# Performance work log

Measured on AMD Instinct MI355X. Metric: run time of the kernel, lower is better.

The kernel has to match this reference:

```python
import jax, jax.numpy as jnp
import numpy as np
import math

D_MODEL = 64
N_HEAD = 8
BATCH = 16
NTOK = 511  # pads to 512 in original torch code; padn = 1 > 0


def setup_inputs() -> dict:
    key = jax.random.key(0)
    ks = jax.random.split(key, 4)
    scl = 0.005
    x = jax.random.normal(ks[0], (BATCH, NTOK, D_MODEL), jnp.float32)
    wq_w = scl * jax.random.normal(ks[1], (N_HEAD * D_MODEL, D_MODEL + 1), jnp.float32)
    wq_w = wq_w.at[:, -1].set(0.0)  # bias column zeroed at init
    wv_w = scl * jax.random.normal(ks[2], (N_HEAD * D_MODEL, D_MODEL + 1), jnp.float32)
    wv_w = wv_w.at[:, -1].set(0.0)
    wk = scl * jnp.ones((N_HEAD, D_MODEL), jnp.float32)
    fanout_w = scl * jax.random.normal(ks[3], (D_MODEL, D_MODEL + 1), jnp.float32)
    fanout_w = fanout_w.at[:, -1].set(0.0)
    return {"x": x, "wq_w": wq_w, "wv_w": wv_w, "wk": wk, "fanout_w": fanout_w}


def _linear_m(w, x):
    # LinearM: w[:, :-1] is weight, w[:, -1] is bias
    return jnp.einsum('oi,bti->bto', w[:, :-1], x) + w[:, -1]


def _l1_logits(q, k):
    # q, k: [b, t, h, w]. Returns [b, s(key), d(query), h] =
    #   -(1/sqrt(w)) * sum_w |q[b,d,h,w] - k[b,s,h,w]|
    # Scan over the width axis so we never materialize a [b,t,t,h,w] tensor.
    b, t, h, w = q.shape
    scale = 1.0 / math.sqrt(w)
    qw = jnp.moveaxis(q, -1, 0)  # [w, b, t, h]
    kw = jnp.moveaxis(k, -1, 0)

    def body(acc, qk):
        qi, ki = qk  # each [b, t, h]
        return acc + jnp.abs(qi[:, None, :, :] - ki[:, :, None, :]), None

    acc0 = jnp.zeros((b, t, t, h), q.dtype)
    acc, _ = jax.lax.scan(body, acc0, (qw, kw))
    return -acc * scale


def reference(x, wq_w, wv_w, wk, fanout_w):
    b, t, dm = x.shape
    q = _linear_m(wq_w, x).reshape(b, t, N_HEAD, D_MODEL)
    v = _linear_m(wv_w, x).reshape(b, t, N_HEAD, D_MODEL)
    # k: x broadcast over heads, elementwise-gated by wk
    k = x[:, :, None, :] * wk[None, None, :, :]  # [b, t, h, w]
    logits = _l1_logits(q, k)  # [b, s, d, h]
    # Extra zero-logit 'sink' key row (the original zero-padded row with a[:,t,:,:]=0)
    sink = jnp.zeros((b, 1, t, N_HEAD), logits.dtype)
    logits = jnp.concatenate([logits, sink], axis=1)  # [b, t+1, d, h]
    a = jax.nn.softmax(logits, axis=1)[:, :t]  # softmax over keys+sink, drop sink
    # einsum 'bsdh,bshw->bdhw' then sum over h, fused:
    out = jnp.einsum('bsdh,bshw->bdw', a, v)  # [b, t, d_model]
    y = jax.nn.relu(out)  # module's self.gelu is actually nn.ReLU()
    y = _linear_m(fanout_w, y)
    return x + y
```

## Files before the change

kernel.cpp:

```cpp
#include <hip/hip_runtime.h>
#include <stdint.h>


#define B  16
#define H  8
#define T  511

typedef __fp16 f16x2 __attribute__((ext_vector_type(2)));
typedef __fp16 f16x8 __attribute__((ext_vector_type(8)));
typedef float  f32x4 __attribute__((ext_vector_type(4)));

#if __has_builtin(__builtin_amdgcn_exp2f)
#define EXP2F(x) __builtin_amdgcn_exp2f(x)
#else
#define EXP2F(x) exp2f(x)
#endif

__device__ __forceinline__ uint32_t SAD(uint32_t a, uint32_t b, uint32_t c) {
#if __has_builtin(__builtin_amdgcn_sad_u8)
  return __builtin_amdgcn_sad_u8(a, b, c);
#else
  uint32_t d;
  asm("v_sad_u8 %0, %1, %2, %3" : "=v"(d) : "v"(a), "v"(b), "v"(c));
  return d;
#endif
}

__device__ __forceinline__ uint32_t PKRTZ(float a, float b) {
  f16x2 r = __builtin_amdgcn_cvt_pkrtz(a, b);
  return __builtin_bit_cast(uint32_t, r);
}

__device__ __forceinline__ uint32_t quantu8(float v) {
  float q = __builtin_rintf(__builtin_fmaf(v, 256.f, 128.f));
  q = fminf(fmaxf(q, 0.f), 255.f);
  return (uint32_t)(int)q;
}

__global__ void wtrans_kernel(const float* __restrict__ wq, const float* __restrict__ wv,
                              const float* __restrict__ wf, float* __restrict__ wt,
                              float* __restrict__ bias, float* __restrict__ wft,
                              float* __restrict__ biasf) {
  const int idx = blockIdx.x * 256 + (int)threadIdx.x;
  if (idx < 64 * 1024) {
    const int k = idx >> 10, j = idx & 1023;
    const float* src = (j < 512) ? wq : wv;
    const int oc = j & 511;
    wt[idx] = src[oc * 65 + k];
    if (k == 0) bias[j] = src[oc * 65 + 64];
  } else if (idx < 64 * 1024 + 64 * 64) {
    const int r = idx - 64 * 1024;
    const int k = r >> 6, w = r & 63;
    wft[r] = wf[w * 65 + k];
    if (k == 0) biasf[w] = wf[w * 65 + 64];
  }
}

__global__ void __launch_bounds__(256, 2) proj_kernel(
    const float* __restrict__ x, const float* __restrict__ wt,
    const float* __restrict__ bias, const float* __restrict__ wk,
    uint8_t* __restrict__ qq, _Float16* __restrict__ vt,
    uint8_t* __restrict__ kq) {
  __shared__ float xt[64][16];
  const int b = blockIdx.y, tc = blockIdx.x;
  const int t0 = tc * 16;
  const int tid = threadIdx.x;
  {
    const int tl = tid >> 4, k0 = (tid & 15) * 4;
    const int t = t0 + tl;
    float4 v = {0.f, 0.f, 0.f, 0.f};
    if (t < T) v = *(const float4*)(x + ((size_t)b * T + t) * 64 + k0);
    xt[k0 + 0][tl] = v.x; xt[k0 + 1][tl] = v.y;
    xt[k0 + 2][tl] = v.z; xt[k0 + 3][tl] = v.w;
  }
  __syncthreads();
  const int j0 = tid * 4;
  const float4 bs = *(const float4*)(bias + j0);
  float4 acc[16];
#pragma unroll
  for (int t = 0; t < 16; ++t) acc[t] = bs;
  for (int k = 0; k < 64; ++k) {
    const float4 w4 = *(const float4*)(wt + (size_t)k * 1024 + j0);
    const float4* xr = (const float4*)xt[k];
    const float4 xa = xr[0], xb = xr[1], xc = xr[2], xd = xr[3];
    const float xv[16] = {xa.x, xa.y, xa.z, xa.w, xb.x, xb.y, xb.z, xb.w,
                          xc.x, xc.y, xc.z, xc.w, xd.x, xd.y, xd.z, xd.w};
#pragma unroll
    for (int t = 0; t < 16; ++t) {
      acc[t].x = __builtin_fmaf(w4.x, xv[t], acc[t].x);
      acc[t].y = __builtin_fmaf(w4.y, xv[t], acc[t].y);
      acc[t].z = __builtin_fmaf(w4.z, xv[t], acc[t].z);
      acc[t].w = __builtin_fmaf(w4.w, xv[t], acc[t].w);
    }
  }
  const int oc = j0 & 511;
  const int hh = oc >> 6, w0 = oc & 63;
  const size_t bh = (size_t)b * H + hh;
  if (j0 < 512) {
#pragma unroll
    for (int t = 0; t < 16; ++t) {
      if (t0 + t < T) {
        const uint32_t u = quantu8(acc[t].x) | (quantu8(acc[t].y) << 8) |
                           (quantu8(acc[t].z) << 16) | (quantu8(acc[t].w) << 24);
        *(uint32_t*)(qq + (bh * T + (size_t)(t0 + t)) * 64 + w0) = u;
      }
    }
  } else {
#pragma unroll
    for (int i = 0; i < 4; ++i) {
      uint32_t u[8];
      const float* a = (const float*)acc;
#pragma unroll
      for (int m = 0; m < 8; ++m) u[m] = PKRTZ(a[4 * (2 * m) + i], a[4 * (2 * m + 1) + i]);
      _Float16* p = vt + (bh * 64 + (size_t)(w0 + i)) * 512 + t0;
      *(uint4*)(p)     = make_uint4(u[0], u[1], u[2], u[3]);
      *(uint4*)(p + 8) = make_uint4(u[4], u[5], u[6], u[7]);
    }
  }
  const int tk = tid >> 4, w4 = (tid & 15) * 4;
  if (t0 + tk < T) {
    const float xv0 = xt[w4 + 0][tk], xv1 = xt[w4 + 1][tk];
    const float xv2 = xt[w4 + 2][tk], xv3 = xt[w4 + 3][tk];
#pragma unroll
    for (int hh2 = 0; hh2 < H; ++hh2) {
      const float4 wkv = *(const float4*)(wk + hh2 * 64 + w4);
      const uint32_t u = quantu8(xv0 * wkv.x) | (quantu8(xv1 * wkv.y) << 8) |
                         (quantu8(xv2 * wkv.z) << 16) | (quantu8(xv3 * wkv.w) << 24);
      *(uint32_t*)(kq + (((size_t)b * H + hh2) * T + (size_t)(t0 + tk)) * 64 + w4) = u;
    }
  }
}

__global__ void __launch_bounds__(256, 4) attn_kernel(
    const uint8_t* __restrict__ qq, const uint8_t* __restrict__ kq,
    const _Float16* __restrict__ vt, _Float16* __restrict__ anum) {
  __shared__ uint4 klds[2048];
  const int qt = blockIdx.x, h = blockIdx.y, b = blockIdx.z;
  const int bh = b * H + h;
  const int tid = threadIdx.x;
  {
    const uint4* kg = (const uint4*)(kq + (size_t)bh * T * 64);
    for (int i = tid; i < T * 4; i += 256) klds[i] = kg[i];
  }
  const int wave = tid >> 6, lane = tid & 63;
  const int c = lane & 15, g = lane >> 4;
  const int qb = qt * 64 + wave * 16;
  const int q = qb + c;
  const int qsafe = q < T ? q : T - 1;
  const uint4* qp = (const uint4*)(qq + ((size_t)bh * T + qsafe) * 64);
  const uint4 q0 = qp[0], q1 = qp[1], q2 = qp[2], q3 = qp[3];
  const _Float16* vb = vt + (size_t)bh * 64 * 512;
  f32x4 acc0 = {0.f, 0.f, 0.f, 0.f}, acc1 = acc0, acc2 = acc0, acc3 = acc0;
  float den = 0.f;
  const float Cl = -0x1.715476p+0f / 2048.0f;
  __syncthreads();

  auto sadrow = [&](int s) -> float {
    const uint4* kp = klds + s * 4;
    const uint4 k0 = kp[0], k1 = kp[1], k2 = kp[2], k3 = kp[3];
    uint32_t a0 = 0, a1 = 0;
    a0 = SAD(q0.x, k0.x, a0); a0 = SAD(q0.y, k0.y, a0);
    a0 = SAD(q0.z, k0.z, a0); a0 = SAD(q0.w, k0.w, a0);
    a0 = SAD(q1.x, k1.x, a0); a0 = SAD(q1.y, k1.y, a0);
    a0 = SAD(q1.z, k1.z, a0); a0 = SAD(q1.w, k1.w, a0);
    a1 = SAD(q2.x, k2.x, a1); a1 = SAD(q2.y, k2.y, a1);
    a1 = SAD(q2.z, k2.z, a1); a1 = SAD(q2.w, k2.w, a1);
    a1 = SAD(q3.x, k3.x, a1); a1 = SAD(q3.y, k3.y, a1);
    a1 = SAD(q3.z, k3.z, a1); a1 = SAD(q3.w, k3.w, a1);
    return EXP2F((float)(a0 + a1) * Cl);
  };

  for (int kt = 0; kt < 16; ++kt) {
    const int ks = kt * 32;
    const _Float16* vp0 = vb + (size_t)c * 512 + ks + g * 8;
    uint4 bvec[4];
#pragma unroll
    for (int nt = 0; nt < 4; ++nt) bvec[nt] = *(const uint4*)(vp0 + nt * 16 * 512);
    uint32_t pk[4];
#pragma unroll
    for (int jj = 0; jj < 4; ++jj) {
      float pp[2];
#pragma unroll
      for (int e = 0; e < 2; ++e) {
        const int s = ks + g * 8 + jj * 2 + e;
        const float p = sadrow(s < T ? s : T - 1);
        pp[e] = (s < T) ? p : 0.f;
      }
      den += pp[0] + pp[1];
      pk[jj] = PKRTZ(pp[0], pp[1]);
    }
    const f16x8 af = __builtin_bit_cast(f16x8, make_uint4(pk[0], pk[1], pk[2], pk[3]));
#pragma unroll
    for (int nt = 0; nt < 4; ++nt) {
      const f16x8 bf = __builtin_bit_cast(f16x8, bvec[nt]);
      switch (nt) {
        case 0: acc0 = __builtin_amdgcn_mfma_f32_16x16x32_f16(af, bf, acc0, 0, 0, 0); break;
        case 1: acc1 = __builtin_amdgcn_mfma_f32_16x16x32_f16(af, bf, acc1, 0, 0, 0); break;
        case 2: acc2 = __builtin_amdgcn_mfma_f32_16x16x32_f16(af, bf, acc2, 0, 0, 0); break;
        case 3: acc3 = __builtin_amdgcn_mfma_f32_16x16x32_f16(af, bf, acc3, 0, 0, 0); break;
      }
    }
  }

  den += __shfl_xor(den, 16, 64);
  den += __shfl_xor(den, 32, 64);
  den += 1.0f;
  float rd[4];
#pragma unroll
  for (int r = 0; r < 4; ++r) rd[r] = 1.0f / __shfl(den, g * 4 + r, 64);
#pragma unroll
  for (int r = 0; r < 4; ++r) {
    const int qr = qb + g * 4 + r;
    if (qr < T) {
      _Float16* ap = anum + (((size_t)b * T + qr) * H + h) * 64 + c;
      ap[0]  = (_Float16)(acc0[r] * rd[r]);
      ap[16] = (_Float16)(acc1[r] * rd[r]);
      ap[32] = (_Float16)(acc2[r] * rd[r]);
      ap[48] = (_Float16)(acc3[r] * rd[r]);
    }
  }
}

__global__ void __launch_bounds__(256) finalize_kernel(
    const float* __restrict__ x, const _Float16* __restrict__ anum,
    const float* __restrict__ wft, const float* __restrict__ biasf,
    float* __restrict__ out) {
  __shared__ float u[4][64];
  const int tid = threadIdx.x;
  const int lt = tid >> 6, w = tid & 63;
  const int gt = blockIdx.x * 4 + lt;
  const _Float16* an = anum + (size_t)gt * H * 64 + w;
  float s = 0.f;
#pragma unroll
  for (int hh = 0; hh < H; ++hh) s += (float)an[hh * 64];
  u[lt][w] = fmaxf(s, 0.f);
  __syncthreads();
  float y = biasf[w];
#pragma unroll 8
  for (int k = 0; k < 64; ++k) y = __builtin_fmaf(wft[k * 64 + w], u[lt][k], y);
  out[(size_t)gt * 64 + w] = x[(size_t)gt * 64 + w] + y;
}

extern "C" void kernel_launch(void* const* d_in, const int* in_sizes, int n_in,
                              void* d_out, int out_size, void* d_ws, size_t ws_size,
                              hipStream_t stream) {
  (void)in_sizes; (void)n_in; (void)out_size; (void)ws_size;
  const float* x  = (const float*)d_in[0];
  const float* wq = (const float*)d_in[1];
  const float* wv = (const float*)d_in[2];
  const float* wk = (const float*)d_in[3];
  const float* wf = (const float*)d_in[4];
  float* out = (float*)d_out;

  uint8_t* ws = (uint8_t*)d_ws;
  const size_t o_qq   = 0;
  const size_t o_kq   = 4186112;
  const size_t o_vt   = 8372224;
  const size_t o_anum = 16760832;
  const size_t o_wt   = 25133056;
  const size_t o_bias = 25395200;
  const size_t o_wft  = 25399296;
  const size_t o_bf   = 25415680;

  uint8_t*  qq    = ws + o_qq;
  uint8_t*  kq    = ws + o_kq;
  _Float16* vt    = (_Float16*)(ws + o_vt);
  _Float16* anum  = (_Float16*)(ws + o_anum);
  float*    wt    = (float*)(ws + o_wt);
  float*    bias  = (float*)(ws + o_bias);
  float*    wft   = (float*)(ws + o_wft);
  float*    biasf = (float*)(ws + o_bf);

  wtrans_kernel<<<dim3((64 * 1024 + 64 * 64 + 255) / 256), 256, 0, stream>>>(
      wq, wv, wf, wt, bias, wft, biasf);
  proj_kernel<<<dim3(32, B), 256, 0, stream>>>(x, wt, bias, wk, qq, vt, kq);
  attn_kernel<<<dim3(8, H, B), 256, 0, stream>>>(qq, kq, vt, anum);
  finalize_kernel<<<dim3(B * T / 4), 256, 0, stream>>>(x, anum, wft, biasf, out);
}
```

Measured before the change: 78.77 us.

## Process four query tiles per wave to reuse K loads and V fragments

```diff
diff --git a/kernel.cpp b/kernel.cpp
--- a/kernel.cpp
+++ b/kernel.cpp
@@ -131,7 +131,7 @@
   }
 }
 
-__global__ void __launch_bounds__(256, 4) attn_kernel(
+__global__ void __launch_bounds__(256, 1) attn_kernel(
     const uint8_t* __restrict__ qq, const uint8_t* __restrict__ kq,
     const _Float16* __restrict__ vt, _Float16* __restrict__ anum) {
   __shared__ uint4 klds[2048];
@@ -140,83 +140,103 @@
   const int tid = threadIdx.x;
   {
     const uint4* kg = (const uint4*)(kq + (size_t)bh * T * 64);
-    for (int i = tid; i < T * 4; i += 256) klds[i] = kg[i];
+    for (int i = tid; i < T * 4; i += 256) {
+      const int s = i >> 2, j = i & 3;
+      klds[s * 4 + (j ^ ((s >> 3) & 3))] = kg[i];
+    }
   }
   const int wave = tid >> 6, lane = tid & 63;
   const int c = lane & 15, g = lane >> 4;
-  const int qb = qt * 64 + wave * 16;
-  const int q = qb + c;
-  const int qsafe = q < T ? q : T - 1;
-  const uint4* qp = (const uint4*)(qq + ((size_t)bh * T + qsafe) * 64);
-  const uint4 q0 = qp[0], q1 = qp[1], q2 = qp[2], q3 = qp[3];
+  const int qb = qt * 256 + wave * 64;
+  uint4 q[4][4];
+#pragma unroll
+  for (int m = 0; m < 4; ++m) {
+    const int qm = qb + 16 * m + c;
+    const int qsafe = qm < T ? qm : T - 1;
+    const uint4* qp = (const uint4*)(qq + ((size_t)bh * T + qsafe) * 64);
+#pragma unroll
+    for (int i = 0; i < 4; ++i) q[m][i] = qp[i];
+  }
   const _Float16* vb = vt + (size_t)bh * 64 * 512;
-  f32x4 acc0 = {0.f, 0.f, 0.f, 0.f}, acc1 = acc0, acc2 = acc0, acc3 = acc0;
-  float den = 0.f;
+  f32x4 acc[4][4];
+#pragma unroll
+  for (int m = 0; m < 4; ++m)
+#pragma unroll
+    for (int nt = 0; nt < 4; ++nt) acc[m][nt] = f32x4{0.f, 0.f, 0.f, 0.f};
+  float den[4] = {0.f, 0.f, 0.f, 0.f};
   const float Cl = -0x1.715476p+0f / 2048.0f;
   __syncthreads();
 
-  auto sadrow = [&](int s) -> float {
-    const uint4* kp = klds + s * 4;
-    const uint4 k0 = kp[0], k1 = kp[1], k2 = kp[2], k3 = kp[3];
-    uint32_t a0 = 0, a1 = 0;
-    a0 = SAD(q0.x, k0.x, a0); a0 = SAD(q0.y, k0.y, a0);
-    a0 = SAD(q0.z, k0.z, a0); a0 = SAD(q0.w, k0.w, a0);
-    a0 = SAD(q1.x, k1.x, a0); a0 = SAD(q1.y, k1.y, a0);
-    a0 = SAD(q1.z, k1.z, a0); a0 = SAD(q1.w, k1.w, a0);
-    a1 = SAD(q2.x, k2.x, a1); a1 = SAD(q2.y, k2.y, a1);
-    a1 = SAD(q2.z, k2.z, a1); a1 = SAD(q2.w, k2.w, a1);
-    a1 = SAD(q3.x, k3.x, a1); a1 = SAD(q3.y, k3.y, a1);
-    a1 = SAD(q3.z, k3.z, a1); a1 = SAD(q3.w, k3.w, a1);
-    return EXP2F((float)(a0 + a1) * Cl);
-  };
-
+#pragma unroll 1
   for (int kt = 0; kt < 16; ++kt) {
     const int ks = kt * 32;
     const _Float16* vp0 = vb + (size_t)c * 512 + ks + g * 8;
     uint4 bvec[4];
 #pragma unroll
     for (int nt = 0; nt < 4; ++nt) bvec[nt] = *(const uint4*)(vp0 + nt * 16 * 512);
-    uint32_t pk[4];
+    uint32_t pk[4][4];
 #pragma unroll
     for (int jj = 0; jj < 4; ++jj) {
-      float pp[2];
+      float pp[4][2];
 #pragma unroll
       for (int e = 0; e < 2; ++e) {
         const int s = ks + g * 8 + jj * 2 + e;
-        const float p = sadrow(s < T ? s : T - 1);
-        pp[e] = (s < T) ? p : 0.f;
-      }
-      den += pp[0] + pp[1];
-      pk[jj] = PKRTZ(pp[0], pp[1]);
-    }
-    const f16x8 af = __builtin_bit_cast(f16x8, make_uint4(pk[0], pk[1], pk[2], pk[3]));
-#pragma unroll
-    for (int nt = 0; nt < 4; ++nt) {
-      const f16x8 bf = __builtin_bit_cast(f16x8, bvec[nt]);
-      switch (nt) {
-        case 0: acc0 = __builtin_amdgcn_mfma_f32_16x16x32_f16(af, bf, acc0, 0, 0, 0); break;
-        case 1: acc1 = __builtin_amdgcn_mfma_f32_16x16x32_f16(af, bf, acc1, 0, 0, 0); break;
-        case 2: acc2 = __builtin_amdgcn_mfma_f32_16x16x32_f16(af, bf, acc2, 0, 0, 0); break;
-        case 3: acc3 = __builtin_amdgcn_mfma_f32_16x16x32_f16(af, bf, acc3, 0, 0, 0); break;
-      }
-    }
-  }
-
-  den += __shfl_xor(den, 16, 64);
-  den += __shfl_xor(den, 32, 64);
-  den += 1.0f;
-  float rd[4];
-#pragma unroll
-  for (int r = 0; r < 4; ++r) rd[r] = 1.0f / __shfl(den, g * 4 + r, 64);
-#pragma unroll
-  for (int r = 0; r < 4; ++r) {
-    const int qr = qb + g * 4 + r;
-    if (qr < T) {
-      _Float16* ap = anum + (((size_t)b * T + qr) * H + h) * 64 + c;
-      ap[0]  = (_Float16)(acc0[r] * rd[r]);
-      ap[16] = (_Float16)(acc1[r] * rd[r]);
-      ap[32] = (_Float16)(acc2[r] * rd[r]);
-      ap[48] = (_Float16)(acc3[r] * rd[r]);
+        const int sr = s < T ? s : T - 1;
+        const uint4* kp = klds + sr * 4;
+        const int bb = (sr >> 3) & 3;
+        const uint4 k0 = kp[bb], k1 = kp[1 ^ bb], k2 = kp[2 ^ bb], k3 = kp[3 ^ bb];
+        const bool live = s < T;
+#pragma unroll
+        for (int m = 0; m < 4; ++m) {
+          uint32_t a0 = 0, a1 = 0;
+          a0 = SAD(q[m][0].x, k0.x, a0); a0 = SAD(q[m][0].y, k0.y, a0);
+          a0 = SAD(q[m][0].z, k0.z, a0); a0 = SAD(q[m][0].w, k0.w, a0);
+          a0 = SAD(q[m][1].x, k1.x, a0); a0 = SAD(q[m][1].y, k1.y, a0);
+          a0 = SAD(q[m][1].z, k1.z, a0); a0 = SAD(q[m][1].w, k1.w, a0);
+          a1 = SAD(q[m][2].x, k2.x, a1); a1 = SAD(q[m][2].y, k2.y, a1);
+          a1 = SAD(q[m][2].z, k2.z, a1); a1 = SAD(q[m][2].w, k2.w, a1);
+          a1 = SAD(q[m][3].x, k3.x, a1); a1 = SAD(q[m][3].y, k3.y, a1);
+          a1 = SAD(q[m][3].z, k3.z, a1); a1 = SAD(q[m][3].w, k3.w, a1);
+          const float p = EXP2F((float)(a0 + a1) * Cl);
+          pp[m][e] = live ? p : 0.f;
+        }
+      }
+#pragma unroll
+      for (int m = 0; m < 4; ++m) {
+        den[m] += pp[m][0] + pp[m][1];
+        pk[m][jj] = PKRTZ(pp[m][0], pp[m][1]);
+      }
+    }
+#pragma unroll
+    for (int m = 0; m < 4; ++m) {
+      const f16x8 af = __builtin_bit_cast(f16x8, make_uint4(pk[m][0], pk[m][1], pk[m][2], pk[m][3]));
+#pragma unroll
+      for (int nt = 0; nt < 4; ++nt) {
+        const f16x8 bf = __builtin_bit_cast(f16x8, bvec[nt]);
+        acc[m][nt] = __builtin_amdgcn_mfma_f32_16x16x32_f16(af, bf, acc[m][nt], 0, 0, 0);
+      }
+    }
+  }
+
+#pragma unroll
+  for (int m = 0; m < 4; ++m) {
+    den[m] += __shfl_xor(den[m], 16, 64);
+    den[m] += __shfl_xor(den[m], 32, 64);
+    den[m] += 1.0f;
+  }
+#pragma unroll
+  for (int m = 0; m < 4; ++m) {
+#pragma unroll
+    for (int r = 0; r < 4; ++r) {
+      const float rd = 1.0f / __shfl(den[m], g * 4 + r, 64);
+      const int qr = qb + 16 * m + g * 4 + r;
+      if (qr < T) {
+        _Float16* ap = anum + (((size_t)b * T + qr) * H + h) * 64 + c;
+        ap[0]  = (_Float16)(acc[m][0][r] * rd);
+        ap[16] = (_Float16)(acc[m][1][r] * rd);
+        ap[32] = (_Float16)(acc[m][2][r] * rd);
+        ap[48] = (_Float16)(acc[m][3][r] * rd);
+      }
     }
   }
 }
@@ -274,6 +294,6 @@
   wtrans_kernel<<<dim3((64 * 1024 + 64 * 64 + 255) / 256), 256, 0, stream>>>(
       wq, wv, wf, wt, bias, wft, biasf);
   proj_kernel<<<dim3(32, B), 256, 0, stream>>>(x, wt, bias, wk, qq, vt, kq);
-  attn_kernel<<<dim3(8, H, B), 256, 0, stream>>>(qq, kq, vt, anum);
+  attn_kernel<<<dim3(2, H, B), 256, 0, stream>>>(qq, kq, vt, anum);
   finalize_kernel<<<dim3(B * T / 4), 256, 0, stream>>>(x, anum, wft, biasf, out);
 }
```

New measurement: 76.52 us. 1.03x faster.
